# Kernel tuning notes

Measured on AMD Instinct MI355X. Metric: run time of the kernel, lower is better.

The kernel has to match this reference:

```python
import jax, jax.numpy as jnp
import numpy as np

IN_DIM = 768
OUT_DIM = 768


def setup_inputs() -> dict:
    key = jax.random.key(0)
    k_x, k_q, k_k, k_v = jax.random.split(key, 4)
    B, S = 4, 4096
    x = jax.random.normal(k_x, (B, S, IN_DIM), dtype=jnp.float32)
    scale = 1.0 / np.sqrt(IN_DIM)
    Wq = jax.random.normal(k_q, (IN_DIM, OUT_DIM), dtype=jnp.float32) * scale
    Wk = jax.random.normal(k_k, (IN_DIM, OUT_DIM), dtype=jnp.float32) * scale
    Wv = jax.random.normal(k_v, (IN_DIM, OUT_DIM), dtype=jnp.float32) * scale
    return {"x": x, "Wq": Wq, "Wk": Wk, "Wv": Wv}


def reference(x, Wq, Wk, Wv):
    # x: [B, S, D_in]; W*: [D_in, D_out] (Linear without bias)
    q = jnp.einsum('bsd,de->bse', x, Wq)
    k = jnp.einsum('bsd,de->bse', x, Wk)
    v = jnp.einsum('bsd,de->bse', x, Wv)
    S = x.shape[1]
    scores = jnp.einsum('bqe,bke->bqk', q, k)  # [B, S, S]
    causal = jnp.tril(jnp.ones((S, S), dtype=bool))  # True where allowed
    scores = jnp.where(causal[None], scores, -jnp.inf)
    scale = 1.0 / jnp.sqrt(jnp.asarray(q.shape[-1], dtype=scores.dtype))
    weights = jax.nn.softmax(scores * scale, axis=-1)
    # dropout p=0.0 -> identity
    return jnp.einsum('bqk,bke->bqe', weights, v)
```

## Files before the change

### kernel.cpp

```cpp
#include <hip/hip_runtime.h>
#include <hip/hip_bf16.h>
#include <hip/hip_fp16.h>

#define DIM 768
#define SLEN 4096
#define BATCH 4
#define NTILES 528

typedef __attribute__((ext_vector_type(8))) short short8;
typedef __attribute__((ext_vector_type(4))) short short4v;
typedef __attribute__((ext_vector_type(4))) float f32x4;
typedef __attribute__((ext_vector_type(8))) _Float16 f16x8;

typedef __attribute__((address_space(1))) void gvoid;
typedef __attribute__((address_space(3))) void lvoid;

__device__ __forceinline__ void gl_lds16(const void* g, void* l) {
  __builtin_amdgcn_global_load_lds((gvoid*)g, (lvoid*)l, 16, 0, 0);
}

__device__ __forceinline__ unsigned short f2h(float x) {
  union { _Float16 h; unsigned short u; } c; c.h = (_Float16)x; return c.u;
}
__device__ __forceinline__ float h2f(unsigned short u) {
  union { _Float16 h; unsigned short u; } c; c.u = u; return (float)c.h;
}

union V8 { short8 v; unsigned short u[8]; };

__global__ __launch_bounds__(256) void convert_x_kernel(
    const float* __restrict__ x, unsigned short* __restrict__ xb) {
  size_t i = ((size_t)blockIdx.x * 256 + threadIdx.x) * 8;
  f32x4 a = *(const f32x4*)(x + i);
  f32x4 b = *(const f32x4*)(x + i + 4);
  V8 o;
#pragma unroll
  for (int j = 0; j < 4; ++j) { o.u[j] = f2h(a[j]); o.u[4 + j] = f2h(b[j]); }
  *(short8*)(xb + i) = o.v;
}

__global__ __launch_bounds__(256) void transpose_w_kernel(
    const float* __restrict__ Wq, const float* __restrict__ Wk,
    const float* __restrict__ Wv, unsigned short* __restrict__ Wt) {
  __shared__ float Tl[32][33];
  const float* Wi = blockIdx.z == 0 ? Wq : (blockIdx.z == 1 ? Wk : Wv);
  unsigned short* Wo = Wt + (size_t)blockIdx.z * DIM * DIM;
  int k0 = blockIdx.x * 32, n0 = blockIdx.y * 32;
  int t = threadIdx.x;
  int r = t >> 3, c4 = (t & 7) * 4;
  f32x4 v = *(const f32x4*)(Wi + (size_t)(k0 + r) * DIM + n0 + c4);
#pragma unroll
  for (int j = 0; j < 4; ++j) Tl[r][c4 + j] = v[j];
  __syncthreads();
  short4v ov;
#pragma unroll
  for (int j = 0; j < 4; ++j) ov[j] = (short)f2h(Tl[c4 + j][r]);
  *(short4v*)(Wo + (size_t)(n0 + r) * DIM + k0 + c4) = ov;
}

__global__ __launch_bounds__(256) void gemm_qkv_kernel(
    const unsigned short* __restrict__ xb, const unsigned short* __restrict__ wt,
    unsigned short* __restrict__ Qo, unsigned short* __restrict__ Ko,
    unsigned short* __restrict__ Vt) {
  __shared__ __align__(16) unsigned short lds[128 * 136];
  unsigned short* As = lds;
  unsigned short* Bs = lds + 4096;
  const int t = threadIdx.x, lane = t & 63, w = t >> 6;
  const int l15 = lane & 15, lg = lane >> 4;
  const int wm = w >> 1, wn = w & 1;
  const int m0 = blockIdx.x * 128, n0 = blockIdx.y * 128;
  const int z = blockIdx.z;
  const unsigned short* B = wt + (size_t)z * DIM * DIM;
  f32x4 acc[4][4];
#pragma unroll
  for (int a = 0; a < 4; ++a)
#pragma unroll
    for (int b2 = 0; b2 < 4; ++b2) acc[a][b2] = f32x4{0.f, 0.f, 0.f, 0.f};
  const int c0 = t, c1 = t + 256;
  const int r0 = c0 >> 2, k80 = (c0 & 3) * 8;
  const int r1 = c1 >> 2, k81 = (c1 & 3) * 8;

  for (int kb = 0; kb < DIM; kb += 32) {
    __syncthreads();
    gl_lds16(xb + (size_t)(m0 + r0) * DIM + kb + k80, As + (size_t)c0 * 8);
    gl_lds16(xb + (size_t)(m0 + r1) * DIM + kb + k81, As + (size_t)c1 * 8);
    gl_lds16(B + (size_t)(n0 + r0) * DIM + kb + k80, Bs + (size_t)c0 * 8);
    gl_lds16(B + (size_t)(n0 + r1) * DIM + kb + k81, Bs + (size_t)c1 * 8);
    __syncthreads();
    f16x8 a[4], bf[4];
#pragma unroll
    for (int mi = 0; mi < 4; ++mi)
      a[mi] = __builtin_bit_cast(f16x8, *(const short8*)(As + (wm * 64 + mi * 16 + l15) * 32 + lg * 8));
#pragma unroll
    for (int ni = 0; ni < 4; ++ni)
      bf[ni] = __builtin_bit_cast(f16x8, *(const short8*)(Bs + (wn * 64 + ni * 16 + l15) * 32 + lg * 8));
#pragma unroll
    for (int mi = 0; mi < 4; ++mi)
#pragma unroll
      for (int ni = 0; ni < 4; ++ni)
        acc[mi][ni] = __builtin_amdgcn_mfma_f32_16x16x32_f16(a[mi], bf[ni], acc[mi][ni], 0, 0, 0);
  }

  if (z < 2) {
    unsigned short* O = (z == 0) ? Qo : Ko;
#pragma unroll
    for (int mi = 0; mi < 4; ++mi)
#pragma unroll
      for (int ni = 0; ni < 4; ++ni)
#pragma unroll
        for (int ii = 0; ii < 4; ++ii) {
          int row = m0 + wm * 64 + mi * 16 + lg * 4 + ii;
          int col = n0 + wn * 64 + ni * 16 + l15;
          O[(size_t)row * DIM + col] = f2h(acc[mi][ni][ii]);
        }
  } else {
    __syncthreads();
    unsigned short* T = lds;
#pragma unroll
    for (int mi = 0; mi < 4; ++mi)
#pragma unroll
      for (int ni = 0; ni < 4; ++ni)
#pragma unroll
        for (int ii = 0; ii < 4; ++ii) {
          int sl = wm * 64 + mi * 16 + lg * 4 + ii;
          int nl = wn * 64 + ni * 16 + l15;
          T[nl * 136 + sl] = f2h(acc[mi][ni][ii]);
        }
    __syncthreads();
    int bidx = m0 >> 12;
    int s0 = m0 & (SLEN - 1);
    unsigned short* O = Vt + (size_t)bidx * DIM * SLEN;
    int nr = t >> 1, hf = t & 1;
#pragma unroll
    for (int j = 0; j < 8; ++j)
      *(short8*)(O + (size_t)(n0 + nr) * SLEN + s0 + hf * 64 + j * 8) =
          *(const short8*)(T + nr * 136 + hf * 64 + j * 8);
  }
}

__global__ __launch_bounds__(256) void gemm_qk_kernel(
    const unsigned short* __restrict__ Q, const unsigned short* __restrict__ K,
    unsigned short* __restrict__ S, size_t qk_bstride, size_t s_bstride) {
  __shared__ __align__(16) unsigned short As[4096], Bs[4096];
  const int i = blockIdx.x, b = blockIdx.y;
  int qt = (int)((sqrtf(8.f * i + 1.f) - 1.f) * 0.5f);
  while ((qt + 1) * (qt + 2) / 2 <= i) ++qt;
  while (qt * (qt + 1) / 2 > i) --qt;
  const int kt = i - qt * (qt + 1) / 2;
  const unsigned short* Qb = Q + (size_t)b * qk_bstride + (size_t)qt * 128 * DIM;
  const unsigned short* Kb = K + (size_t)b * qk_bstride + (size_t)kt * 128 * DIM;
  unsigned short* Sb = S + (size_t)b * s_bstride + (size_t)i * 16384;

  const int t = threadIdx.x, lane = t & 63, w = t >> 6;
  const int l15 = lane & 15, lg = lane >> 4;
  const int wm = w >> 1, wn = w & 1;
  f32x4 acc[4][4];
#pragma unroll
  for (int a = 0; a < 4; ++a)
#pragma unroll
    for (int b2 = 0; b2 < 4; ++b2) acc[a][b2] = f32x4{0.f, 0.f, 0.f, 0.f};
  const int c0 = t, c1 = t + 256;
  const int r0 = c0 >> 2, k80 = (c0 & 3) * 8;
  const int r1 = c1 >> 2, k81 = (c1 & 3) * 8;

  for (int kb = 0; kb < DIM; kb += 32) {
    __syncthreads();
    gl_lds16(Qb + (size_t)r0 * DIM + kb + k80, As + (size_t)c0 * 8);
    gl_lds16(Qb + (size_t)r1 * DIM + kb + k81, As + (size_t)c1 * 8);
    gl_lds16(Kb + (size_t)r0 * DIM + kb + k80, Bs + (size_t)c0 * 8);
    gl_lds16(Kb + (size_t)r1 * DIM + kb + k81, Bs + (size_t)c1 * 8);
    __syncthreads();
    f16x8 a[4], bf[4];
#pragma unroll
    for (int mi = 0; mi < 4; ++mi)
      a[mi] = __builtin_bit_cast(f16x8, *(const short8*)(As + (wm * 64 + mi * 16 + l15) * 32 + lg * 8));
#pragma unroll
    for (int ni = 0; ni < 4; ++ni)
      bf[ni] = __builtin_bit_cast(f16x8, *(const short8*)(Bs + (wn * 64 + ni * 16 + l15) * 32 + lg * 8));
#pragma unroll
    for (int mi = 0; mi < 4; ++mi)
#pragma unroll
      for (int ni = 0; ni < 4; ++ni)
        acc[mi][ni] = __builtin_amdgcn_mfma_f32_16x16x32_f16(a[mi], bf[ni], acc[mi][ni], 0, 0, 0);
  }
#pragma unroll
  for (int mi = 0; mi < 4; ++mi)
#pragma unroll
    for (int ni = 0; ni < 4; ++ni)
#pragma unroll
      for (int ii = 0; ii < 4; ++ii) {
        int rl = wm * 64 + mi * 16 + lg * 4 + ii;
        int cl = wn * 64 + ni * 16 + l15;
        Sb[rl * 128 + cl] = f2h(acc[mi][ni][ii]);
      }
}

__global__ __launch_bounds__(256) void softmax_kernel(
    unsigned short* __restrict__ S, size_t s_bstride) {
  __shared__ float redm[4], reds[4];
  const int r = blockIdx.x, b = blockIdx.y;
  unsigned short* Sb = S + (size_t)b * s_bstride;
  const int qt = r >> 7, rl = r & 127;
  const int ncols = (qt + 1) * 128;
  const size_t rowbase = (size_t)(qt * (qt + 1) / 2) * 16384 + (size_t)rl * 128;
  const int t = threadIdx.x, lane = t & 63, w = t >> 6;
  const int c0 = t * 16;
  const bool act = c0 < ncols;
  const float NEG = -3.0e38f;
  float sv[16];
  unsigned short* p = nullptr;
  if (act) {
    int ktile = c0 >> 7, cl = c0 & 127;
    p = Sb + rowbase + (size_t)ktile * 16384 + cl;
    V8 v0, v1; v0.v = *(const short8*)p; v1.v = *(const short8*)(p + 8);
#pragma unroll
    for (int j = 0; j < 8; ++j) {
      sv[j] = (c0 + j > r) ? NEG : h2f(v0.u[j]);
      sv[8 + j] = (c0 + 8 + j > r) ? NEG : h2f(v1.u[j]);
    }
  } else {
#pragma unroll
    for (int j = 0; j < 16; ++j) sv[j] = NEG;
  }
  float mx = NEG;
#pragma unroll
  for (int j = 0; j < 16; ++j) mx = fmaxf(mx, sv[j]);
#pragma unroll
  for (int d = 1; d < 64; d <<= 1) mx = fmaxf(mx, __shfl_xor(mx, d));
  if (lane == 0) redm[w] = mx;
  __syncthreads();
  mx = fmaxf(fmaxf(redm[0], redm[1]), fmaxf(redm[2], redm[3]));

  const float scl = 1.4426950408889634f / 27.712812921102035f;
  float e[16], sm = 0.f;
#pragma unroll
  for (int j = 0; j < 16; ++j) { e[j] = exp2f((sv[j] - mx) * scl); sm += e[j]; }
#pragma unroll
  for (int d = 1; d < 64; d <<= 1) sm += __shfl_xor(sm, d);
  if (lane == 0) reds[w] = sm;
  __syncthreads();
  float inv = 1.0f / (reds[0] + reds[1] + reds[2] + reds[3]);
  if (act) {
    V8 o0, o1;
#pragma unroll
    for (int j = 0; j < 8; ++j) { o0.u[j] = f2h(e[j] * inv); o1.u[j] = f2h(e[8 + j] * inv); }
    *(short8*)p = o0.v;
    *(short8*)(p + 8) = o1.v;
  }
}

__global__ __launch_bounds__(256) void gemm_pv_kernel(
    const unsigned short* __restrict__ S, const unsigned short* __restrict__ Vt,
    float* __restrict__ Out, size_t s_bstride, int nb) {
  __shared__ __align__(16) unsigned short As[4096], Bs[4096];
  const int idx = blockIdx.x;
  const int qtr = idx / (6 * nb);
  const int rem = idx - qtr * 6 * nb;
  const int b = rem / 6, nt = rem % 6;
  const int qt = 31 - qtr;
  const unsigned short* Sb = S + (size_t)b * s_bstride + (size_t)(qt * (qt + 1) / 2) * 16384;
  const unsigned short* Vb = Vt + (size_t)b * DIM * SLEN + (size_t)(nt * 128) * SLEN;
  float* Ob = Out + (size_t)b * SLEN * DIM + (size_t)(qt * 128) * DIM + nt * 128;

  const int t = threadIdx.x, lane = t & 63, w = t >> 6;
  const int l15 = lane & 15, lg = lane >> 4;
  const int wm = w >> 1, wn = w & 1;
  f32x4 acc[4][4];
#pragma unroll
  for (int a = 0; a < 4; ++a)
#pragma unroll
    for (int b2 = 0; b2 < 4; ++b2) acc[a][b2] = f32x4{0.f, 0.f, 0.f, 0.f};
  const int c0 = t, c1 = t + 256;
  const int r0 = c0 >> 2, k80 = (c0 & 3) * 8;
  const int r1 = c1 >> 2, k81 = (c1 & 3) * 8;

  const int ksteps = (qt + 1) * 4;
  for (int ks = 0; ks < ksteps; ++ks) {
    const int kb = ks * 32;
    const size_t atile = (size_t)(kb >> 7) * 16384 + (size_t)(kb & 127);
    __syncthreads();
    gl_lds16(Sb + atile + (size_t)r0 * 128 + k80, As + (size_t)c0 * 8);
    gl_lds16(Sb + atile + (size_t)r1 * 128 + k81, As + (size_t)c1 * 8);
    gl_lds16(Vb + (size_t)r0 * SLEN + kb + k80, Bs + (size_t)c0 * 8);
    gl_lds16(Vb + (size_t)r1 * SLEN + kb + k81, Bs + (size_t)c1 * 8);
    __syncthreads();
    f16x8 a[4], bf[4];
#pragma unroll
    for (int mi = 0; mi < 4; ++mi)
      a[mi] = __builtin_bit_cast(f16x8, *(const short8*)(As + (wm * 64 + mi * 16 + l15) * 32 + lg * 8));
#pragma unroll
    for (int ni = 0; ni < 4; ++ni)
      bf[ni] = __builtin_bit_cast(f16x8, *(const short8*)(Bs + (wn * 64 + ni * 16 + l15) * 32 + lg * 8));
#pragma unroll
    for (int mi = 0; mi < 4; ++mi)
#pragma unroll
      for (int ni = 0; ni < 4; ++ni)
        acc[mi][ni] = __builtin_amdgcn_mfma_f32_16x16x32_f16(a[mi], bf[ni], acc[mi][ni], 0, 0, 0);
  }
#pragma unroll
  for (int mi = 0; mi < 4; ++mi)
#pragma unroll
    for (int ni = 0; ni < 4; ++ni)
#pragma unroll
      for (int ii = 0; ii < 4; ++ii) {
        int rl = wm * 64 + mi * 16 + lg * 4 + ii;
        int cl = wn * 64 + ni * 16 + l15;
        Ob[(size_t)rl * DIM + cl] = acc[mi][ni][ii];
      }
}

extern "C" void kernel_launch(void* const* d_in, const int* in_sizes, int n_in,
                              void* d_out, int out_size, void* d_ws, size_t ws_size,
                              hipStream_t stream) {
  const float* x  = (const float*)d_in[0];
  const float* Wq = (const float*)d_in[1];
  const float* Wk = (const float*)d_in[2];
  const float* Wv = (const float*)d_in[3];
  float* out = (float*)d_out;

  const size_t n_x = (size_t)BATCH * SLEN * DIM;
  const size_t S_PB = (size_t)NTILES * 16384;
  unsigned short* Q  = (unsigned short*)d_ws;
  unsigned short* K  = Q + n_x;
  unsigned short* Vt = K + n_x;
  unsigned short* xb = Vt + n_x;
  unsigned short* wt = xb + n_x;
  const size_t base_elems = 4 * n_x + (size_t)3 * DIM * DIM;
  const bool full = ws_size >= (base_elems + 4 * S_PB) * 2;

  convert_x_kernel<<<dim3((unsigned)(n_x / 8 / 256)), 256, 0, stream>>>(x, xb);
  transpose_w_kernel<<<dim3(DIM / 32, DIM / 32, 3), 256, 0, stream>>>(Wq, Wk, Wv, wt);
  gemm_qkv_kernel<<<dim3((BATCH * SLEN) / 128, DIM / 128, 3), 256, 0, stream>>>(
      xb, wt, Q, K, Vt);

  if (full) {
    unsigned short* S = (unsigned short*)d_ws + base_elems;
    gemm_qk_kernel<<<dim3(NTILES, BATCH), 256, 0, stream>>>(
        Q, K, S, (size_t)SLEN * DIM, S_PB);
    softmax_kernel<<<dim3(SLEN, BATCH), 256, 0, stream>>>(S, S_PB);
    gemm_pv_kernel<<<dim3(32 * 6 * BATCH), 256, 0, stream>>>(S, Vt, out, S_PB, BATCH);
  } else {
    unsigned short* S = xb;
    for (int b = 0; b < BATCH; ++b) {
      const size_t qo = (size_t)b * SLEN * DIM;
      gemm_qk_kernel<<<dim3(NTILES, 1), 256, 0, stream>>>(Q + qo, K + qo, S, 0, 0);
      softmax_kernel<<<dim3(SLEN, 1), 256, 0, stream>>>(S, 0);
      gemm_pv_kernel<<<dim3(32 * 6), 256, 0, stream>>>(
          S, Vt + (size_t)b * DIM * SLEN, out + qo, 0, 1);
    }
  }
}
```

Before: 327.4 us.

## Use 256x256 pipelined 8-wave GEMM for QKV and QK^T with swizzled LDS

Replaces the 128x128 single-buffered QKV and QK^T GEMMs with a 512-thread 256x256 tile kernel. It double-buffers LDS loads with global_load_lds, applies an XOR swizzle to avoid bank conflicts, and interleaves MFMA phases with raised wave priority. V is now written row-major and transposed by a separate kernel. The larger tiles cut global traffic per FLOP and hide load latency. The cost is an extra transpose pass and wasted compute on diagonal 256 tiles whose upper halves are skipped at store time.

```diff
diff --git a/kernel.cpp b/kernel.cpp
--- a/kernel.cpp
+++ b/kernel.cpp
@@ -6,6 +6,7 @@
 #define SLEN 4096
 #define BATCH 4
 #define NTILES 528
+#define NT256 136
 
 typedef __attribute__((ext_vector_type(8))) short short8;
 typedef __attribute__((ext_vector_type(4))) short short4v;
@@ -58,9 +59,165 @@
   *(short4v*)(Wo + (size_t)(n0 + r) * DIM + k0 + c4) = ov;
 }
 
-__global__ __launch_bounds__(256) void gemm_qkv_kernel(
+
+#define STAGE(src, row0, kb, ldsoff)                                              \
+  {                                                                               \
+    gl_lds16((src) + (size_t)((row0) + rA) * DIM + (kb) + cA,                     \
+             ldsb + (ldsoff) + t * 16);                                           \
+    gl_lds16((src) + (size_t)((row0) + 64 + rA) * DIM + (kb) + cA,                \
+             ldsb + (ldsoff) + 8192 + t * 16);                                    \
+  }
+
+#define QPHASE(MH, CHB, STG, VMW)                                                 \
+  {                                                                               \
+    f16x8 afr[4];                                                                 \
+    _Pragma("unroll") for (int j = 0; j < 4; ++j)                                 \
+        afr[j] = __builtin_bit_cast(f16x8, *(const short8*)(ldsb + aB +           \
+                 (MH) * 16384 + (j * 32 + arow) * 128 + (CHB)));                  \
+    if ((MH) == 0) {                                                              \
+      _Pragma("unroll") for (int n = 0; n < 4; ++n)                               \
+          bfr[n] = __builtin_bit_cast(f16x8, *(const short8*)(ldsb + bB +         \
+                   bh * 16384 + (brow + n * 16) * 128 + (CHB)));                  \
+    }                                                                             \
+    STG;                                                                          \
+    VMW;                                                                          \
+    asm volatile("s_barrier" ::: "memory");                                       \
+    asm volatile("s_waitcnt lgkmcnt(0)" ::: "memory");                            \
+    __builtin_amdgcn_sched_barrier(0);                                            \
+    __builtin_amdgcn_s_setprio(1);                                                \
+    _Pragma("unroll") for (int j = 0; j < 4; ++j)                                 \
+      _Pragma("unroll") for (int n = 0; n < 4; ++n)                               \
+        acc[(MH) * 4 + j][n] = __builtin_amdgcn_mfma_f32_16x16x32_f16(            \
+            afr[j], bfr[n], acc[(MH) * 4 + j][n], 0, 0, 0);                       \
+    __builtin_amdgcn_s_setprio(0);                                                \
+    __builtin_amdgcn_sched_barrier(0);                                            \
+    asm volatile("s_barrier" ::: "memory");                                       \
+  }
+
+template <int MODE>
+__global__ __launch_bounds__(512, 2) void gemm8_kernel(
+    const unsigned short* __restrict__ Ag, const unsigned short* __restrict__ Bg,
+    unsigned short* __restrict__ o0, unsigned short* __restrict__ o1,
+    unsigned short* __restrict__ o2, size_t stAB, size_t stS) {
+  __shared__ __align__(16) unsigned short lds[65536];
+  char* ldsb = (char*)lds;
+  const int t = threadIdx.x;
+  const int lane = t & 63, w = t >> 6;
+  const int l15 = lane & 15, lg = lane >> 4;
+  const int wr = w >> 2, wc = w & 3;
+
+  int m0, n0, qt = 0, kt = 0;
+  const unsigned short *A, *B;
+  unsigned short* Co = nullptr;
+  unsigned short* Sb = nullptr;
+  if (MODE == 0) {
+    m0 = blockIdx.x * 256; n0 = blockIdx.y * 256;
+    A = Ag; B = Bg + (size_t)blockIdx.z * DIM * DIM;
+    Co = blockIdx.z == 0 ? o0 : (blockIdx.z == 1 ? o1 : o2);
+  } else {
+    const int i = blockIdx.x, b = blockIdx.y;
+    qt = (int)((sqrtf(8.f * i + 1.f) - 1.f) * 0.5f);
+    while ((qt + 1) * (qt + 2) / 2 <= i) ++qt;
+    while (qt * (qt + 1) / 2 > i) --qt;
+    kt = i - qt * (qt + 1) / 2;
+    m0 = qt * 256; n0 = kt * 256;
+    A = Ag + (size_t)b * stAB; B = Bg + (size_t)b * stAB;
+    Sb = o0 + (size_t)b * stS;
+  }
+
+  const int rA = t >> 3;
+  const int cA = (((t & 7) ^ ((t >> 3) & 7)) << 3);
+  const int ch0 = ((lg ^ (l15 & 7)) << 4);
+  const int arow = wr * 16 + l15;
+  const int bh = wc >> 1;
+  const int brow = (wc & 1) * 64 + l15;
+
+  f32x4 acc[8][4];
+#pragma unroll
+  for (int f = 0; f < 8; ++f)
+#pragma unroll
+    for (int n = 0; n < 4; ++n) acc[f][n] = f32x4{0.f, 0.f, 0.f, 0.f};
+
+  STAGE(A, m0, 0, 0);
+  STAGE(B, n0, 0, 65536);
+  STAGE(B, n0 + 128, 0, 65536 + 16384);
+  STAGE(A, m0 + 128, 0, 16384);
+  STAGE(A, m0, 64, 32768);
+  asm volatile("s_waitcnt vmcnt(4)" ::: "memory");
+  asm volatile("s_barrier" ::: "memory");
+
+  for (int tt = 0; tt < 12; ++tt) {
+    const int bt = tt & 1;
+    const int aB = bt * 32768;
+    const int bB = 65536 + bt * 32768;
+    const int aN = (1 - bt) * 32768;
+    const int bN = 65536 + (1 - bt) * 32768;
+    const int kb1 = (tt + 1 < 12 ? tt + 1 : 11) * 64;
+    const int kb2 = (tt + 2 < 12 ? tt + 2 : 11) * 64;
+    f16x8 bfr[4];
+    QPHASE(0, ch0, STAGE(B, n0, kb1, bN),
+           asm volatile("s_waitcnt vmcnt(4)" ::: "memory"));
+    QPHASE(1, ch0, STAGE(B, n0 + 128, kb1, bN + 16384), (void)0);
+    QPHASE(0, ch0 ^ 64, STAGE(A, m0 + 128, kb1, aN + 16384), (void)0);
+    QPHASE(1, ch0 ^ 64, STAGE(A, m0, kb2, aB),
+           asm volatile("s_waitcnt vmcnt(4)" ::: "memory"));
+  }
+  asm volatile("s_waitcnt vmcnt(0)" ::: "memory");
+
+  if (MODE == 0) {
+#pragma unroll
+    for (int f = 0; f < 8; ++f) {
+      const int row = m0 + f * 32 + wr * 16 + lg * 4;
+#pragma unroll
+      for (int n = 0; n < 4; ++n) {
+        const int col = n0 + wc * 64 + n * 16 + l15;
+#pragma unroll
+        for (int ii = 0; ii < 4; ++ii)
+          Co[(size_t)(row + ii) * DIM + col] = f2h(acc[f][n][ii]);
+      }
+    }
+  } else {
+#pragma unroll
+    for (int f = 0; f < 8; ++f) {
+      const int rl = (f * 32 + wr * 16 + lg * 4) & 127;
+      const int Q128 = qt * 2 + (f >= 4 ? 1 : 0);
+      const int K128 = kt * 2 + (wc >> 1);
+      if (K128 > Q128) continue;
+      const size_t tb = (size_t)(Q128 * (Q128 + 1) / 2 + K128) * 16384;
+#pragma unroll
+      for (int n = 0; n < 4; ++n) {
+        const int cl = ((wc & 1) * 64 + n * 16 + l15);
+#pragma unroll
+        for (int ii = 0; ii < 4; ++ii)
+          Sb[tb + (size_t)(rl + ii) * 128 + cl] = f2h(acc[f][n][ii]);
+      }
+    }
+  }
+}
+
+__global__ __launch_bounds__(256) void transpose_v_kernel(
+    const unsigned short* __restrict__ Vn, unsigned short* __restrict__ Vt) {
+  __shared__ unsigned short T[64][72];
+  const int s0 = blockIdx.x * 64, e0 = blockIdx.y * 64;
+  const size_t bo = (size_t)blockIdx.z * SLEN * DIM;
+  const int t = threadIdx.x;
+  const int r = t >> 2, c = (t & 3) * 16;
+  V8 v0, v1;
+  v0.v = *(const short8*)(Vn + bo + (size_t)(s0 + r) * DIM + e0 + c);
+  v1.v = *(const short8*)(Vn + bo + (size_t)(s0 + r) * DIM + e0 + c + 8);
+#pragma unroll
+  for (int j = 0; j < 8; ++j) { T[r][c + j] = v0.u[j]; T[r][c + 8 + j] = v1.u[j]; }
+  __syncthreads();
+  unsigned short* Ob = Vt + (size_t)blockIdx.z * DIM * SLEN;
+  V8 o0, o1;
+#pragma unroll
+  for (int j = 0; j < 8; ++j) { o0.u[j] = T[c + j][r]; o1.u[j] = T[c + 8 + j][r]; }
+  *(short8*)(Ob + (size_t)(e0 + r) * SLEN + s0 + c) = o0.v;
+  *(short8*)(Ob + (size_t)(e0 + r) * SLEN + s0 + c + 8) = o1.v;
+}
+
+__global__ __launch_bounds__(256) void gemm_v128_kernel(
     const unsigned short* __restrict__ xb, const unsigned short* __restrict__ wt,
-    unsigned short* __restrict__ Qo, unsigned short* __restrict__ Ko,
     unsigned short* __restrict__ Vt) {
   __shared__ __align__(16) unsigned short lds[128 * 136];
   unsigned short* As = lds;
@@ -69,8 +226,7 @@
   const int l15 = lane & 15, lg = lane >> 4;
   const int wm = w >> 1, wn = w & 1;
   const int m0 = blockIdx.x * 128, n0 = blockIdx.y * 128;
-  const int z = blockIdx.z;
-  const unsigned short* B = wt + (size_t)z * DIM * DIM;
+  const unsigned short* B = wt + (size_t)2 * DIM * DIM;
   f32x4 acc[4][4];
 #pragma unroll
   for (int a = 0; a < 4; ++a)
@@ -79,7 +235,6 @@
   const int c0 = t, c1 = t + 256;
   const int r0 = c0 >> 2, k80 = (c0 & 3) * 8;
   const int r1 = c1 >> 2, k81 = (c1 & 3) * 8;
-
   for (int kb = 0; kb < DIM; kb += 32) {
     __syncthreads();
     gl_lds16(xb + (size_t)(m0 + r0) * DIM + kb + k80, As + (size_t)c0 * 8);
@@ -100,99 +255,27 @@
       for (int ni = 0; ni < 4; ++ni)
         acc[mi][ni] = __builtin_amdgcn_mfma_f32_16x16x32_f16(a[mi], bf[ni], acc[mi][ni], 0, 0, 0);
   }
-
-  if (z < 2) {
-    unsigned short* O = (z == 0) ? Qo : Ko;
-#pragma unroll
-    for (int mi = 0; mi < 4; ++mi)
-#pragma unroll
-      for (int ni = 0; ni < 4; ++ni)
-#pragma unroll
-        for (int ii = 0; ii < 4; ++ii) {
-          int row = m0 + wm * 64 + mi * 16 + lg * 4 + ii;
-          int col = n0 + wn * 64 + ni * 16 + l15;
-          O[(size_t)row * DIM + col] = f2h(acc[mi][ni][ii]);
-        }
-  } else {
-    __syncthreads();
-    unsigned short* T = lds;
-#pragma unroll
-    for (int mi = 0; mi < 4; ++mi)
-#pragma unroll
-      for (int ni = 0; ni < 4; ++ni)
-#pragma unroll
-        for (int ii = 0; ii < 4; ++ii) {
-          int sl = wm * 64 + mi * 16 + lg * 4 + ii;
-          int nl = wn * 64 + ni * 16 + l15;
-          T[nl * 136 + sl] = f2h(acc[mi][ni][ii]);
-        }
-    __syncthreads();
-    int bidx = m0 >> 12;
-    int s0 = m0 & (SLEN - 1);
-    unsigned short* O = Vt + (size_t)bidx * DIM * SLEN;
-    int nr = t >> 1, hf = t & 1;
-#pragma unroll
-    for (int j = 0; j < 8; ++j)
-      *(short8*)(O + (size_t)(n0 + nr) * SLEN + s0 + hf * 64 + j * 8) =
-          *(const short8*)(T + nr * 136 + hf * 64 + j * 8);
-  }
-}
-
-__global__ __launch_bounds__(256) void gemm_qk_kernel(
-    const unsigned short* __restrict__ Q, const unsigned short* __restrict__ K,
-    unsigned short* __restrict__ S, size_t qk_bstride, size_t s_bstride) {
-  __shared__ __align__(16) unsigned short As[4096], Bs[4096];
-  const int i = blockIdx.x, b = blockIdx.y;
-  int qt = (int)((sqrtf(8.f * i + 1.f) - 1.f) * 0.5f);
-  while ((qt + 1) * (qt + 2) / 2 <= i) ++qt;
-  while (qt * (qt + 1) / 2 > i) --qt;
-  const int kt = i - qt * (qt + 1) / 2;
-  const unsigned short* Qb = Q + (size_t)b * qk_bstride + (size_t)qt * 128 * DIM;
-  const unsigned short* Kb = K + (size_t)b * qk_bstride + (size_t)kt * 128 * DIM;
-  unsigned short* Sb = S + (size_t)b * s_bstride + (size_t)i * 16384;
-
-  const int t = threadIdx.x, lane = t & 63, w = t >> 6;
-  const int l15 = lane & 15, lg = lane >> 4;
-  const int wm = w >> 1, wn = w & 1;
-  f32x4 acc[4][4];
-#pragma unroll
-  for (int a = 0; a < 4; ++a)
-#pragma unroll
-    for (int b2 = 0; b2 < 4; ++b2) acc[a][b2] = f32x4{0.f, 0.f, 0.f, 0.f};
-  const int c0 = t, c1 = t + 256;
-  const int r0 = c0 >> 2, k80 = (c0 & 3) * 8;
-  const int r1 = c1 >> 2, k81 = (c1 & 3) * 8;
-
-  for (int kb = 0; kb < DIM; kb += 32) {
-    __syncthreads();
-    gl_lds16(Qb + (size_t)r0 * DIM + kb + k80, As + (size_t)c0 * 8);
-    gl_lds16(Qb + (size_t)r1 * DIM + kb + k81, As + (size_t)c1 * 8);
-    gl_lds16(Kb + (size_t)r0 * DIM + kb + k80, Bs + (size_t)c0 * 8);
-    gl_lds16(Kb + (size_t)r1 * DIM + kb + k81, Bs + (size_t)c1 * 8);
-    __syncthreads();
-    f16x8 a[4], bf[4];
-#pragma unroll
-    for (int mi = 0; mi < 4; ++mi)
-      a[mi] = __builtin_bit_cast(f16x8, *(const short8*)(As + (wm * 64 + mi * 16 + l15) * 32 + lg * 8));
+  __syncthreads();
+  unsigned short* T = lds;
+#pragma unroll
+  for (int mi = 0; mi < 4; ++mi)
 #pragma unroll
     for (int ni = 0; ni < 4; ++ni)
-      bf[ni] = __builtin_bit_cast(f16x8, *(const short8*)(Bs + (wn * 64 + ni * 16 + l15) * 32 + lg * 8));
-#pragma unroll
-    for (int mi = 0; mi < 4; ++mi)
-#pragma unroll
-      for (int ni = 0; ni < 4; ++ni)
-        acc[mi][ni] = __builtin_amdgcn_mfma_f32_16x16x32_f16(a[mi], bf[ni], acc[mi][ni], 0, 0, 0);
-  }
-#pragma unroll
-  for (int mi = 0; mi < 4; ++mi)
-#pragma unroll
-    for (int ni = 0; ni < 4; ++ni)
 #pragma unroll
       for (int ii = 0; ii < 4; ++ii) {
-        int rl = wm * 64 + mi * 16 + lg * 4 + ii;
-        int cl = wn * 64 + ni * 16 + l15;
-        Sb[rl * 128 + cl] = f2h(acc[mi][ni][ii]);
+        int sl = wm * 64 + mi * 16 + lg * 4 + ii;
+        int nl = wn * 64 + ni * 16 + l15;
+        T[nl * 136 + sl] = f2h(acc[mi][ni][ii]);
       }
+  __syncthreads();
+  int bidx = m0 >> 12;
+  int s0 = m0 & (SLEN - 1);
+  unsigned short* O = Vt + (size_t)bidx * DIM * SLEN;
+  int nr = t >> 1, hf = t & 1;
+#pragma unroll
+  for (int j = 0; j < 8; ++j)
+    *(short8*)(O + (size_t)(n0 + nr) * SLEN + s0 + hf * 64 + j * 8) =
+        *(const short8*)(T + nr * 136 + hf * 64 + j * 8);
 }
 
 __global__ __launch_bounds__(256) void softmax_kernel(
@@ -230,7 +313,6 @@
   if (lane == 0) redm[w] = mx;
   __syncthreads();
   mx = fmaxf(fmaxf(redm[0], redm[1]), fmaxf(redm[2], redm[3]));
-
   const float scl = 1.4426950408889634f / 27.712812921102035f;
   float e[16], sm = 0.f;
 #pragma unroll
@@ -261,7 +343,6 @@
   const unsigned short* Sb = S + (size_t)b * s_bstride + (size_t)(qt * (qt + 1) / 2) * 16384;
   const unsigned short* Vb = Vt + (size_t)b * DIM * SLEN + (size_t)(nt * 128) * SLEN;
   float* Ob = Out + (size_t)b * SLEN * DIM + (size_t)(qt * 128) * DIM + nt * 128;
-
   const int t = threadIdx.x, lane = t & 63, w = t >> 6;
   const int l15 = lane & 15, lg = lane >> 4;
   const int wm = w >> 1, wn = w & 1;
@@ -273,7 +354,6 @@
   const int c0 = t, c1 = t + 256;
   const int r0 = c0 >> 2, k80 = (c0 & 3) * 8;
   const int r1 = c1 >> 2, k81 = (c1 & 3) * 8;
-
   const int ksteps = (qt + 1) * 4;
   for (int ks = 0; ks < ksteps; ++ks) {
     const int kb = ks * 32;
@@ -330,20 +410,24 @@
 
   convert_x_kernel<<<dim3((unsigned)(n_x / 8 / 256)), 256, 0, stream>>>(x, xb);
   transpose_w_kernel<<<dim3(DIM / 32, DIM / 32, 3), 256, 0, stream>>>(Wq, Wk, Wv, wt);
-  gemm_qkv_kernel<<<dim3((BATCH * SLEN) / 128, DIM / 128, 3), 256, 0, stream>>>(
-      xb, wt, Q, K, Vt);
 
   if (full) {
     unsigned short* S = (unsigned short*)d_ws + base_elems;
-    gemm_qk_kernel<<<dim3(NTILES, BATCH), 256, 0, stream>>>(
-        Q, K, S, (size_t)SLEN * DIM, S_PB);
+    unsigned short* Vn = S;
+    gemm8_kernel<0><<<dim3(64, 3, 3), 512, 0, stream>>>(xb, wt, Q, K, Vn, 0, 0);
+    transpose_v_kernel<<<dim3(SLEN / 64, DIM / 64, BATCH), 256, 0, stream>>>(Vn, Vt);
+    gemm8_kernel<1><<<dim3(NT256, BATCH), 512, 0, stream>>>(
+        Q, K, S, nullptr, nullptr, (size_t)SLEN * DIM, S_PB);
     softmax_kernel<<<dim3(SLEN, BATCH), 256, 0, stream>>>(S, S_PB);
     gemm_pv_kernel<<<dim3(32 * 6 * BATCH), 256, 0, stream>>>(S, Vt, out, S_PB, BATCH);
   } else {
+    gemm8_kernel<0><<<dim3(64, 3, 2), 512, 0, stream>>>(xb, wt, Q, K, nullptr, 0, 0);
+    gemm_v128_kernel<<<dim3((BATCH * SLEN) / 128, DIM / 128), 256, 0, stream>>>(xb, wt, Vt);
     unsigned short* S = xb;
     for (int b = 0; b < BATCH; ++b) {
       const size_t qo = (size_t)b * SLEN * DIM;
-      gemm_qk_kernel<<<dim3(NTILES, 1), 256, 0, stream>>>(Q + qo, K + qo, S, 0, 0);
+      gemm8_kernel<1><<<dim3(NT256, 1), 512, 0, stream>>>(
+          Q + qo, K + qo, S, nullptr, nullptr, 0, 0);
       softmax_kernel<<<dim3(SLEN, 1), 256, 0, stream>>>(S, 0);
       gemm_pv_kernel<<<dim3(32 * 6), 256, 0, stream>>>(
           S, Vt + (size_t)b * DIM * SLEN, out + qo, 0, 1);
```

Result: slower. 341.2 us (+4.2%).
